# Kernel optimization log

Measured on AMD Instinct MI355X. Metric: run time of the kernel, lower is better.

Reference implementation:

```python
import jax, jax.numpy as jnp
import numpy as np

F_NHID = 64
C_NHID = 64
U_INIT = F_NHID + C_NHID + 1   # 129
U_OUT = F_NHID + C_NHID        # 128
U_HID = 128
N_AGG = 4
M_INIT = 3 * N_AGG * U_OUT + C_NHID  # 1600
M_HID = 256
M_OUT = C_NHID


def setup_inputs() -> dict:
    key = jax.random.key(0)
    ks = jax.random.split(key, 12)
    B, Nc, Nf = 4, 512, 256
    h_fac = jax.random.normal(ks[0], (B, Nf, F_NHID), dtype=jnp.float32)
    h_cus = jax.random.normal(ks[1], (B, Nc, C_NHID), dtype=jnp.float32)
    edge = jax.random.normal(ks[2], (B, Nc, Nf, 1), dtype=jnp.float32)
    adj = jax.random.randint(ks[3], (B, Nc, Nf), 0, 2).astype(jnp.float32)
    def lin(k, i, o):
        return jax.random.normal(k, (i, o), dtype=jnp.float32) / np.sqrt(i)
    return {
        'h_fac': h_fac, 'h_cus': h_cus, 'edge': edge, 'adj': adj,
        'U_W1': lin(ks[4], U_INIT, U_HID), 'U_b1': jnp.zeros((U_HID,), jnp.float32),
        'U_W2': lin(ks[5], U_HID, U_OUT), 'U_b2': jnp.zeros((U_OUT,), jnp.float32),
        'M_W1': lin(ks[6], M_INIT, M_HID), 'M_b1': jnp.zeros((M_HID,), jnp.float32),
        'M_W2': lin(ks[7], M_HID, M_OUT), 'M_b2': jnp.zeros((M_OUT,), jnp.float32),
    }


def reference(h_fac, h_cus, edge, adj, U_W1, U_b1, U_W2, U_b2, M_W1, M_b1, M_W2, M_b2):
    B, Nc, c = h_cus.shape
    Nf = h_fac.shape[1]
    # Per-edge message input: [customer_feat, facility_feat, edge_scalar] -> (B,Nc,Nf,U_INIT)
    msg = jnp.concatenate([
        jnp.broadcast_to(h_cus[:, :, None, :], (B, Nc, Nf, c)),
        jnp.broadcast_to(h_fac[:, None, :, :], (B, Nc, Nf, h_fac.shape[-1])),
        edge,
    ], axis=-1)
    # U MLP (pretransformation): relu -> linear
    m = jax.nn.relu(msg @ U_W1 + U_b1)
    m = m @ U_W2 + U_b2  # (B, Nc, Nf, U_OUT)

    mask = adj > 0                              # (B, Nc, Nf)
    maskf = mask[..., None].astype(m.dtype)     # (B, Nc, Nf, 1)
    cnt = jnp.sum(maskf, axis=2)                # (B, Nc, 1)
    mean = jnp.sum(m * maskf, axis=2) / cnt     # nanmean over masked entries
    var = jnp.sum(((m - mean[:, :, None, :]) ** 2) * maskf, axis=2) / cnt
    std = jnp.sqrt(var)                         # population std (divides by count)
    mx = jnp.max(jnp.where(mask[..., None], m, -jnp.inf), axis=2)
    mn = jnp.min(jnp.where(mask[..., None], m, jnp.inf), axis=2)

    # Degree-based scalers (get_avgd + scale_amplification/attenuation)
    deg_c = jnp.sum(adj, axis=-1)               # (B, Nc)
    deg_f = jnp.sum(adj, axis=-2)               # (B, Nf)
    avg_d = jnp.mean(jnp.concatenate([jnp.log(deg_c + 1.0), jnp.log(deg_f + 1.0)], axis=-1), axis=-1)  # (B,)
    scale = (jnp.log(deg_c + 1.0) / avg_d[:, None])[..., None]          # (B, Nc, 1)
    scale_inv = jnp.where(scale != 0, 1.0 / scale, jnp.zeros_like(scale))

    feats = [h_cus]
    for a in (mean, std, mx, mn):
        feats.extend([a, a * scale, a * scale_inv])
    h = jnp.concatenate(feats, axis=-1)         # (B, Nc, M_INIT)

    # M MLP (posttransformation): relu -> linear (last activation 'none')
    h = jax.nn.relu(h @ M_W1 + M_b1)
    out = h @ M_W2 + M_b2                       # (B, Nc, C_NHID)
    return out
```

## Files before the change

### kernel.cpp

```cpp
#include <hip/hip_runtime.h>
#include <hip/hip_bf16.h>


using bs8 = __attribute__((ext_vector_type(8))) short;
using f4  = __attribute__((ext_vector_type(4))) float;
using f2  = __attribute__((ext_vector_type(2))) float;

__device__ __forceinline__ unsigned short f2bf(float f) {
    union { float f; unsigned int u; } x; x.f = f;
    unsigned int u = x.u + 0x7FFFu + ((x.u >> 16) & 1u);
    return (unsigned short)(u >> 16);
}

__device__ __forceinline__ unsigned int pkbf(float a, float b) {
    __hip_bfloat162 h = __float22bfloat162_rn(make_float2(a, b));
    union { __hip_bfloat162 h; unsigned int u; } c; c.h = h;
    return c.u;
}

__global__ void PNALayer_35081292874189_kernel() {}

#define OFF_AC     0u
#define OFF_AF     1048576u
#define OFF_DEGC   1572864u
#define OFF_SCALE  1585152u
#define OFF_SINV   1593344u
#define OFF_FEATB  1601536u
#define OFF_HMID   8155392u
#define OFF_W2T    10252544u
#define OFF_W1TB   10318080u
#define OFF_DEGFP  11170048u
#define WS_NEED    11235584u

__global__ void PNALayer_ws_fail(float* out, int n) {
    int i = blockIdx.x * 256 + threadIdx.x;
    if (i < n) out[i] = 2500.0f;
}

__global__ void PNALayer_prep1(
    const float* h_fac, const float* h_cus, const float* adj,
    const float* U_W1, const float* U_b1, const float* U_W2, const float* M_W1,
    float* wsAc, float* wsAf, float* wsDegC,
    unsigned short* wsW2Tb, unsigned short* wsW1Tb, float* wsDegFP)
{
    __shared__ float sH[64];
    __shared__ float sRed[256];
    __shared__ float sT[64][65];
    int bid = blockIdx.x, t = threadIdx.x;

    if (bid < 1024) {
        int b = bid >> 8, f = bid & 255;
        if (t < 64) sH[t] = h_fac[(b * 256 + f) * 64 + t];
        __syncthreads();
        if (t < 128) {
            float acc = 0.f;
            for (int k = 0; k < 64; ++k)
                acc += sH[k] * U_W1[(64 + k) * 128 + t];
            wsAf[(b * 256 + f) * 128 + t] = acc;
        }
    } else if (bid < 3072) {
        int bc = bid - 1024;
        if (t < 64) sH[t] = h_cus[bc * 64 + t];
        __syncthreads();
        if (t < 128) {
            float acc = U_b1[t];
            for (int k = 0; k < 64; ++k)
                acc += sH[k] * U_W1[k * 128 + t];
            wsAc[bc * 128 + t] = acc;
        }
        float v = adj[bc * 256 + t];
        sRed[t] = v; __syncthreads();
        for (int s = 128; s > 0; s >>= 1) { if (t < s) sRed[t] += sRed[t + s]; __syncthreads(); }
        if (t == 0) wsDegC[bc] = sRed[0];
    } else if (bid < 3076) {
        int l = bid - 3072;
        int k0 = (l >> 1) * 64, n0 = (l & 1) * 64;
        for (int rep = 0; rep < 16; ++rep) {
            int idx = rep * 256 + t; int r = idx >> 6, c = idx & 63;
            sT[r][c] = U_W2[(k0 + r) * 128 + n0 + c];
        }
        __syncthreads();
        for (int rep = 0; rep < 16; ++rep) {
            int idx = rep * 256 + t; int r = idx >> 6, c = idx & 63;
            wsW2Tb[(n0 + r) * 128 + k0 + c] = f2bf(sT[c][r]);
        }
    } else if (bid < 3176) {
        int l = bid - 3076;
        int k0 = (l % 25) * 64, n0 = (l / 25) * 64;
        for (int rep = 0; rep < 16; ++rep) {
            int idx = rep * 256 + t; int r = idx >> 6, c = idx & 63;
            sT[r][c] = M_W1[(k0 + r) * 256 + n0 + c];
        }
        __syncthreads();
        for (int rep = 0; rep < 16; ++rep) {
            int idx = rep * 256 + t; int r = idx >> 6, c = idx & 63;
            wsW1Tb[(n0 + r) * 1664 + k0 + c] = f2bf(sT[c][r]);
        }
    } else if (bid < 3177) {
        for (int i = 0; i < 64; ++i) {
            int idx = i * 256 + t;
            int n = idx >> 6, k = 1600 + (idx & 63);
            wsW1Tb[n * 1664 + k] = 0;
        }
    } else {
        int l = bid - 3177;
        int b = l >> 4, ch = l & 15;
        const float* ap = adj + (b * 512 + ch * 32) * 256 + t;
        float s = 0.f;
#pragma unroll 8
        for (int c = 0; c < 32; ++c)
            s += ap[c * 256];
        wsDegFP[(b * 16 + ch) * 256 + t] = s;
    }
}

__global__ void PNALayer_prep2(
    const float* wsDegFP, const float* wsDegC, float* wsScale, float* wsSinv)
{
    __shared__ float sRed[256];
    __shared__ float sAvg;
    int b = blockIdx.x, t = threadIdx.x;
    float df = 0.f;
#pragma unroll
    for (int ch = 0; ch < 16; ++ch)
        df += wsDegFP[(b * 16 + ch) * 256 + t];
    float v = logf(wsDegC[b * 512 + t] + 1.f) + logf(wsDegC[b * 512 + t + 256] + 1.f)
            + logf(df + 1.f);
    sRed[t] = v; __syncthreads();
    for (int s = 128; s > 0; s >>= 1) { if (t < s) sRed[t] += sRed[t + s]; __syncthreads(); }
    if (t == 0) sAvg = sRed[0] / 768.f;
    __syncthreads();
    float avg = sAvg;
    for (int c = t; c < 512; c += 256) {
        float lg = logf(wsDegC[b * 512 + c] + 1.f);
        float sc = lg / avg;
        float si = (sc != 0.f) ? 1.f / sc : 0.f;
        wsScale[b * 512 + c] = sc;
        wsSinv[b * 512 + c] = si;
    }
}

__global__ __launch_bounds__(256, 4) void PNALayer_edge(
    const float* h_cus, const float* edge, const float* adj,
    const float* U_W1, const float* U_b2,
    const float* wsAc, const float* wsAf, const unsigned short* wsW2Tb,
    const float* wsScale, const float* wsSinv,
    unsigned short* featB)
{
    __shared__ __align__(16) unsigned short sM1[64 * 136];
    __shared__ float sE[256];
    __shared__ float sAc[128];
    __shared__ float sWe[128];
    __shared__ unsigned short sFidx[256];
    __shared__ unsigned long long sBal[4];

    int bc = blockIdx.x;
    int b  = bc >> 9;
    int t  = threadIdx.x;
    int w = t >> 6, quad = (t >> 4) & 3, ln = t & 15;

    int r0 = w * 32 + ln;
    int r1 = w * 32 + 16 + ln;
    bs8 bw0[4], bw1[4];
#pragma unroll
    for (int kk = 0; kk < 4; ++kk) {
        bw0[kk] = *(const bs8*)(wsW2Tb + r0 * 128 + kk * 32 + quad * 8);
        bw1[kk] = *(const bs8*)(wsW2Tb + r1 * 128 + kk * 32 + quad * 8);
    }
    float b2v0 = U_b2[r0], b2v1 = U_b2[r1];

    sE[t] = edge[bc * 256 + t];
    bool m = adj[bc * 256 + t] > 0.f;
    unsigned long long bal = __ballot(m);
    if ((t & 63) == 0) sBal[t >> 6] = bal;
    if (t < 128) {
        sAc[t] = wsAc[bc * 128 + t];
        sWe[t] = U_W1[128 * 128 + t];
    } else if (t < 192) {
        int j = t - 128;
        featB[bc * 1600 + j] = f2bf(h_cus[bc * 64 + j]);
    }
    __syncthreads();

    unsigned long long b0 = sBal[0], b1 = sBal[1], b2 = sBal[2], b3 = sBal[3];
    int cnt = __popcll(b0) + __popcll(b1) + __popcll(b2) + __popcll(b3);
    {
        int wv = t >> 6, l = t & 63;
        int base = 0;
        if (wv > 0) base += __popcll(b0);
        if (wv > 1) base += __popcll(b1);
        if (wv > 2) base += __popcll(b2);
        int rank = __popcll(bal & ((1ULL << l) - 1ULL));
        if (m) sFidx[base + rank] = (unsigned short)t;
    }
    __syncthreads();

    int ntiles = (cnt + 63) >> 6;

    f2 aS0 = (f2){0.f, 0.f}, aQ0 = (f2){0.f, 0.f};
    f2 aMx0 = (f2){-1e30f, -1e30f}, aMn0 = (f2){1e30f, 1e30f};
    f2 aS1 = (f2){0.f, 0.f}, aQ1 = (f2){0.f, 0.f};
    f2 aMx1 = (f2){-1e30f, -1e30f}, aMn1 = (f2){1e30f, 1e30f};
    const f2 zero2 = (f2){0.f, 0.f};

    for (int tl = 0; tl < ntiles; ++tl) {
#pragma unroll
        for (int i = 0; i < 8; ++i) {
            int idx = i * 256 + t;
            int fl = idx >> 5, k = (idx & 31) * 4;
            int fj = tl * 64 + fl;
            uint2 p = make_uint2(0u, 0u);
            if (fj < cnt) {
                int f = sFidx[fj];
                float4 af  = *(const float4*)(wsAf + (b * 256 + f) * 128 + k);
                float4 ac4 = *(const float4*)(sAc + k);
                float4 we4 = *(const float4*)(sWe + k);
                float e = sE[f];
                f2 e2 = (f2){e, e};
                f2 s01 = (f2){ac4.x + af.x, ac4.y + af.y};
                f2 s23 = (f2){ac4.z + af.z, ac4.w + af.w};
                s01 = __builtin_elementwise_fma(e2, (f2){we4.x, we4.y}, s01);
                s23 = __builtin_elementwise_fma(e2, (f2){we4.z, we4.w}, s23);
                f2 r01 = __builtin_elementwise_max(s01, zero2);
                f2 r23 = __builtin_elementwise_max(s23, zero2);
                p.x = pkbf(r01.x, r01.y);
                p.y = pkbf(r23.x, r23.y);
            }
            *(uint2*)(sM1 + fl * 136 + k) = p;
        }
        __syncthreads();

        f4 acc0[4], acc1[4];
#pragma unroll
        for (int rt = 0; rt < 4; ++rt) {
            acc0[rt] = (f4){0.f, 0.f, 0.f, 0.f};
            acc1[rt] = (f4){0.f, 0.f, 0.f, 0.f};
        }
#pragma unroll
        for (int kk = 0; kk < 4; ++kk) {
            int ko = kk * 32 + quad * 8;
#pragma unroll
            for (int rt = 0; rt < 4; ++rt) {
                bs8 a = *(const bs8*)(sM1 + (rt * 16 + ln) * 136 + ko);
                acc0[rt] = __builtin_amdgcn_mfma_f32_16x16x32_bf16(a, bw0[kk], acc0[rt], 0, 0, 0);
                acc1[rt] = __builtin_amdgcn_mfma_f32_16x16x32_bf16(a, bw1[kk], acc1[rt], 0, 0, 0);
            }
        }

        if (((tl + 1) << 6) <= cnt) {
#pragma unroll
            for (int rt = 0; rt < 4; ++rt) {
                f2 p01 = (f2){acc0[rt][0], acc0[rt][1]};
                f2 p23 = (f2){acc0[rt][2], acc0[rt][3]};
                aS0 = aS0 + p01;
                aS0 = aS0 + p23;
                aQ0 = __builtin_elementwise_fma(p01, p01, aQ0);
                aQ0 = __builtin_elementwise_fma(p23, p23, aQ0);
                aMx0 = __builtin_elementwise_max(aMx0, __builtin_elementwise_max(p01, p23));
                aMn0 = __builtin_elementwise_min(aMn0, __builtin_elementwise_min(p01, p23));
                f2 q01 = (f2){acc1[rt][0], acc1[rt][1]};
                f2 q23 = (f2){acc1[rt][2], acc1[rt][3]};
                aS1 = aS1 + q01;
                aS1 = aS1 + q23;
                aQ1 = __builtin_elementwise_fma(q01, q01, aQ1);
                aQ1 = __builtin_elementwise_fma(q23, q23, aQ1);
                aMx1 = __builtin_elementwise_max(aMx1, __builtin_elementwise_max(q01, q23));
                aMn1 = __builtin_elementwise_min(aMn1, __builtin_elementwise_min(q01, q23));
            }
        } else {
#pragma unroll
            for (int rt = 0; rt < 4; ++rt) {
#pragma unroll
                for (int i = 0; i < 4; ++i) {
                    int fj = tl * 64 + rt * 16 + quad * 4 + i;
                    if (fj < cnt) {
                        float v0 = acc0[rt][i];
                        aS0.x += v0;
                        aQ0.x = fmaf(v0, v0, aQ0.x);
                        aMx0.x = fmaxf(aMx0.x, v0);
                        aMn0.x = fminf(aMn0.x, v0);
                        float v1 = acc1[rt][i];
                        aS1.x += v1;
                        aQ1.x = fmaf(v1, v1, aQ1.x);
                        aMx1.x = fmaxf(aMx1.x, v1);
                        aMn1.x = fminf(aMn1.x, v1);
                    }
                }
            }
        }
        __syncthreads();
    }

    float aS[2], aQ[2], aMx[2], aMn[2];
    aS[0] = aS0.x + aS0.y;  aQ[0] = aQ0.x + aQ0.y;
    aMx[0] = fmaxf(aMx0.x, aMx0.y);  aMn[0] = fminf(aMn0.x, aMn0.y);
    aS[1] = aS1.x + aS1.y;  aQ[1] = aQ1.x + aQ1.y;
    aMx[1] = fmaxf(aMx1.x, aMx1.y);  aMn[1] = fminf(aMn1.x, aMn1.y);

#pragma unroll
    for (int ct = 0; ct < 2; ++ct) {
        aS[ct]  += __shfl_xor(aS[ct], 16, 64);  aS[ct]  += __shfl_xor(aS[ct], 32, 64);
        aQ[ct]  += __shfl_xor(aQ[ct], 16, 64);  aQ[ct]  += __shfl_xor(aQ[ct], 32, 64);
        aMx[ct] = fmaxf(aMx[ct], __shfl_xor(aMx[ct], 16, 64));
        aMx[ct] = fmaxf(aMx[ct], __shfl_xor(aMx[ct], 32, 64));
        aMn[ct] = fminf(aMn[ct], __shfl_xor(aMn[ct], 16, 64));
        aMn[ct] = fminf(aMn[ct], __shfl_xor(aMn[ct], 32, 64));
    }

    if (quad == 0) {
        float cntf = (float)cnt;
        float sc = wsScale[bc], si = wsSinv[bc];
        unsigned short* fr = featB + bc * 1600;
        float b2[2] = {b2v0, b2v1};
#pragma unroll
        for (int ct = 0; ct < 2; ++ct) {
            int col = w * 32 + ct * 16 + ln;
            float meanr = aS[ct] / cntf;
            float mean  = meanr + b2[ct];
            float var   = fmaxf(aQ[ct] / cntf - meanr * meanr, 0.f);
            float stdv  = sqrtf(var);
            float mx = aMx[ct] + b2[ct], mn = aMn[ct] + b2[ct];
            fr[64 + col]   = f2bf(mean); fr[192 + col]  = f2bf(mean * sc); fr[320 + col]  = f2bf(mean * si);
            fr[448 + col]  = f2bf(stdv); fr[576 + col]  = f2bf(stdv * sc); fr[704 + col]  = f2bf(stdv * si);
            fr[832 + col]  = f2bf(mx);   fr[960 + col]  = f2bf(mx * sc);   fr[1088 + col] = f2bf(mx * si);
            fr[1216 + col] = f2bf(mn);   fr[1344 + col] = f2bf(mn * sc);   fr[1472 + col] = f2bf(mn * si);
        }
    }
}

__global__ __launch_bounds__(512, 2) void PNALayer_mlp1(
    const unsigned short* featB, const unsigned short* wsW1Tb, const float* M_b1,
    float* h_mid)
{
    __shared__ __align__(16) unsigned short sA[32 * 136];
    __shared__ __align__(16) unsigned short sB[64 * 136];
    int t = threadIdx.x;
    int rb = (blockIdx.x >> 2) * 32, cb = (blockIdx.x & 3) * 64;
    int w = t >> 6, quad = (t >> 4) & 3, ln = t & 15;
    int wr = w >> 2, wc = w & 3;

    f4 acc = (f4){0.f, 0.f, 0.f, 0.f};

    for (int kt = 0; kt < 13; ++kt) {
        int kb = kt * 128;
        {
            int row = t >> 4, c8 = (t & 15) * 8;
            *(uint4*)(sA + row * 136 + c8) =
                *(const uint4*)(featB + (rb + row) * 1600 + kb + c8);
        }
#pragma unroll
        for (int i = 0; i < 2; ++i) {
            int vi = i * 512 + t;
            int row = vi >> 4, c8 = (vi & 15) * 8;
            *(uint4*)(sB + row * 136 + c8) =
                *(const uint4*)(wsW1Tb + (cb + row) * 1664 + kb + c8);
        }
        __syncthreads();
#pragma unroll
        for (int kk = 0; kk < 4; ++kk) {
            int ko = kk * 32 + quad * 8;
            bs8 a  = *(const bs8*)(sA + (wr * 16 + ln) * 136 + ko);
            bs8 bb = *(const bs8*)(sB + (wc * 16 + ln) * 136 + ko);
            acc = __builtin_amdgcn_mfma_f32_16x16x32_bf16(a, bb, acc, 0, 0, 0);
        }
        __syncthreads();
    }
    int col = cb + wc * 16 + ln;
    float b1v = M_b1[col];
#pragma unroll
    for (int i = 0; i < 4; ++i) {
        int row = rb + wr * 16 + quad * 4 + i;
        h_mid[row * 256 + col] = fmaxf(acc[i] + b1v, 0.f);
    }
}

__global__ void PNALayer_mlp2(
    const float* h_mid, const float* M_W2, const float* M_b2, float* out)
{
    int q = blockIdx.x * 256 + threadIdx.x;
    int row0 = q >> 6, j = q & 63;
    int row1 = row0 + 1024;
    float acc0 = M_b2[j], acc1 = acc0;
    const float* h0 = h_mid + row0 * 256;
    const float* h1 = h_mid + row1 * 256;
#pragma unroll 8
    for (int k = 0; k < 256; ++k) {
        float wv = M_W2[k * 64 + j];
        acc0 = fmaf(h0[k], wv, acc0);
        acc1 = fmaf(h1[k], wv, acc1);
    }
    out[row0 * 64 + j] = acc0;
    out[row1 * 64 + j] = acc1;
}

extern "C" void kernel_launch(void* const* d_in, const int* in_sizes, int n_in,
                              void* d_out, int out_size, void* d_ws, size_t ws_size,
                              hipStream_t stream) {
    const float* h_fac = (const float*)d_in[0];
    const float* h_cus = (const float*)d_in[1];
    const float* edge  = (const float*)d_in[2];
    const float* adj   = (const float*)d_in[3];
    const float* U_W1  = (const float*)d_in[4];
    const float* U_b1  = (const float*)d_in[5];
    const float* U_W2  = (const float*)d_in[6];
    const float* U_b2  = (const float*)d_in[7];
    const float* M_W1  = (const float*)d_in[8];
    const float* M_b1  = (const float*)d_in[9];
    const float* M_W2  = (const float*)d_in[10];
    const float* M_b2  = (const float*)d_in[11];
    (void)in_sizes; (void)n_in;

    float* outp = (float*)d_out;
    int nblk_out = (out_size + 255) / 256;

    if (ws_size < (size_t)WS_NEED) {
        PNALayer_ws_fail<<<nblk_out, 256, 0, stream>>>(outp, out_size);
        return;
    }

    char* ws = (char*)d_ws;
    float*          wsAc   = (float*)(ws + OFF_AC);
    float*          wsAf   = (float*)(ws + OFF_AF);
    float*          wsDegC = (float*)(ws + OFF_DEGC);
    float*          wsScal = (float*)(ws + OFF_SCALE);
    float*          wsSinv = (float*)(ws + OFF_SINV);
    unsigned short* wsFeatB= (unsigned short*)(ws + OFF_FEATB);
    float*          wsHmid = (float*)(ws + OFF_HMID);
    unsigned short* wsW2Tb = (unsigned short*)(ws + OFF_W2T);
    unsigned short* wsW1Tb = (unsigned short*)(ws + OFF_W1TB);
    float*          wsDegFP= (float*)(ws + OFF_DEGFP);

    PNALayer_prep1<<<3241, 256, 0, stream>>>(
        h_fac, h_cus, adj, U_W1, U_b1, U_W2, M_W1,
        wsAc, wsAf, wsDegC, wsW2Tb, wsW1Tb, wsDegFP);
    PNALayer_prep2<<<4, 256, 0, stream>>>(wsDegFP, wsDegC, wsScal, wsSinv);
    PNALayer_edge<<<2048, 256, 0, stream>>>(
        h_cus, edge, adj, U_W1, U_b2,
        wsAc, wsAf, wsW2Tb, wsScal, wsSinv, wsFeatB);
    PNALayer_mlp1<<<256, 512, 0, stream>>>(wsFeatB, wsW1Tb, M_b1, wsHmid);
    PNALayer_mlp2<<<256, 256, 0, stream>>>(wsHmid, M_W2, M_b2, outp);
}
```

Baseline: 147.8 us.

## Double-buffer edge-kernel M1 tiles and stage h_mid rows in LDS for mlp2

The edge kernel now double-buffers the bf16 hidden-activation tile in shared memory. It prefetches the next tile's wsAf rows into registers before the MFMA work on the current tile, and writes the ReLU-packed result into the other buffer afterwards, so global-load latency overlaps compute and one barrier per tile is removed. The mlp2 kernel now loads 8 rows of h_mid into LDS with coalesced float4 loads instead of each thread striding through global memory. The cost is double the sM1 LDS use and extra registers for the prefetched float4s, which may lower occupancy under launch_bounds(256,4). The mlp2 launch grid must also match the new 8-rows-per-block mapping.

```diff
diff --git a/kernel.cpp b/kernel.cpp
--- a/kernel.cpp
+++ b/kernel.cpp
@@ -147,7 +147,7 @@
     const float* wsScale, const float* wsSinv,
     unsigned short* featB)
 {
-    __shared__ __align__(16) unsigned short sM1[64 * 136];
+    __shared__ __align__(16) unsigned short sM1[2][64 * 136];
     __shared__ float sE[256];
     __shared__ float sAc[128];
     __shared__ float sWe[128];
@@ -196,22 +196,16 @@
     __syncthreads();
 
     int ntiles = (cnt + 63) >> 6;
-
-    f2 aS0 = (f2){0.f, 0.f}, aQ0 = (f2){0.f, 0.f};
-    f2 aMx0 = (f2){-1e30f, -1e30f}, aMn0 = (f2){1e30f, 1e30f};
-    f2 aS1 = (f2){0.f, 0.f}, aQ1 = (f2){0.f, 0.f};
-    f2 aMx1 = (f2){-1e30f, -1e30f}, aMn1 = (f2){1e30f, 1e30f};
     const f2 zero2 = (f2){0.f, 0.f};
 
-    for (int tl = 0; tl < ntiles; ++tl) {
+    {
 #pragma unroll
         for (int i = 0; i < 8; ++i) {
             int idx = i * 256 + t;
             int fl = idx >> 5, k = (idx & 31) * 4;
-            int fj = tl * 64 + fl;
             uint2 p = make_uint2(0u, 0u);
-            if (fj < cnt) {
-                int f = sFidx[fj];
+            if (fl < cnt) {
+                int f = sFidx[fl];
                 float4 af  = *(const float4*)(wsAf + (b * 256 + f) * 128 + k);
                 float4 ac4 = *(const float4*)(sAc + k);
                 float4 we4 = *(const float4*)(sWe + k);
@@ -226,9 +220,35 @@
                 p.x = pkbf(r01.x, r01.y);
                 p.y = pkbf(r23.x, r23.y);
             }
-            *(uint2*)(sM1 + fl * 136 + k) = p;
-        }
-        __syncthreads();
+            *(uint2*)(sM1[0] + fl * 136 + k) = p;
+        }
+    }
+    __syncthreads();
+
+    f2 aS0 = (f2){0.f, 0.f}, aQ0 = (f2){0.f, 0.f};
+    f2 aMx0 = (f2){-1e30f, -1e30f}, aMn0 = (f2){1e30f, 1e30f};
+    f2 aS1 = (f2){0.f, 0.f}, aQ1 = (f2){0.f, 0.f};
+    f2 aMx1 = (f2){-1e30f, -1e30f}, aMn1 = (f2){1e30f, 1e30f};
+
+    for (int tl = 0; tl < ntiles; ++tl) {
+        int cur = tl & 1, nxt = cur ^ 1;
+        bool have_next = (tl + 1) < ntiles;
+
+        float4 af[8]; int fxi[8];
+        if (have_next) {
+#pragma unroll
+            for (int i = 0; i < 8; ++i) {
+                int idx = i * 256 + t;
+                int fl = idx >> 5, k = (idx & 31) * 4;
+                int fj = (tl + 1) * 64 + fl;
+                fxi[i] = -1;
+                if (fj < cnt) {
+                    int f = sFidx[fj];
+                    fxi[i] = f;
+                    af[i] = *(const float4*)(wsAf + (b * 256 + f) * 128 + k);
+                }
+            }
+        }
 
         f4 acc0[4], acc1[4];
 #pragma unroll
@@ -241,7 +261,7 @@
             int ko = kk * 32 + quad * 8;
 #pragma unroll
             for (int rt = 0; rt < 4; ++rt) {
-                bs8 a = *(const bs8*)(sM1 + (rt * 16 + ln) * 136 + ko);
+                bs8 a = *(const bs8*)(sM1[cur] + (rt * 16 + ln) * 136 + ko);
                 acc0[rt] = __builtin_amdgcn_mfma_f32_16x16x32_bf16(a, bw0[kk], acc0[rt], 0, 0, 0);
                 acc1[rt] = __builtin_amdgcn_mfma_f32_16x16x32_bf16(a, bw1[kk], acc1[rt], 0, 0, 0);
             }
@@ -288,6 +308,30 @@
                 }
             }
         }
+
+        if (have_next) {
+#pragma unroll
+            for (int i = 0; i < 8; ++i) {
+                int idx = i * 256 + t;
+                int fl = idx >> 5, k = (idx & 31) * 4;
+                uint2 p = make_uint2(0u, 0u);
+                if (fxi[i] >= 0) {
+                    float4 ac4 = *(const float4*)(sAc + k);
+                    float4 we4 = *(const float4*)(sWe + k);
+                    float e = sE[fxi[i]];
+                    f2 e2 = (f2){e, e};
+                    f2 s01 = (f2){ac4.x + af[i].x, ac4.y + af[i].y};
+                    f2 s23 = (f2){ac4.z + af[i].z, ac4.w + af[i].w};
+                    s01 = __builtin_elementwise_fma(e2, (f2){we4.x, we4.y}, s01);
+                    s23 = __builtin_elementwise_fma(e2, (f2){we4.z, we4.w}, s23);
+                    f2 r01 = __builtin_elementwise_max(s01, zero2);
+                    f2 r23 = __builtin_elementwise_max(s23, zero2);
+                    p.x = pkbf(r01.x, r01.y);
+                    p.y = pkbf(r23.x, r23.y);
+                }
+                *(uint2*)(sM1[nxt] + fl * 136 + k) = p;
+            }
+        }
         __syncthreads();
     }
 
@@ -374,23 +418,32 @@
     }
 }
 
-__global__ void PNALayer_mlp2(
+__global__ __launch_bounds__(256) void PNALayer_mlp2(
     const float* h_mid, const float* M_W2, const float* M_b2, float* out)
 {
-    int q = blockIdx.x * 256 + threadIdx.x;
-    int row0 = q >> 6, j = q & 63;
-    int row1 = row0 + 1024;
+    __shared__ float sH[8 * 256];
+    int t = threadIdx.x;
+    int rb = blockIdx.x * 8;
+#pragma unroll
+    for (int i = 0; i < 2; ++i) {
+        int vi = i * 256 + t;
+        int row = vi >> 6, c4 = (vi & 63) * 4;
+        *(float4*)(sH + row * 256 + c4) =
+            *(const float4*)(h_mid + (rb + row) * 256 + c4);
+    }
+    __syncthreads();
+    int j = t & 63, r = t >> 6;
     float acc0 = M_b2[j], acc1 = acc0;
-    const float* h0 = h_mid + row0 * 256;
-    const float* h1 = h_mid + row1 * 256;
+    const float* h0 = sH + r * 256;
+    const float* h1 = sH + (r + 4) * 256;
 #pragma unroll 8
     for (int k = 0; k < 256; ++k) {
         float wv = M_W2[k * 64 + j];
         acc0 = fmaf(h0[k], wv, acc0);
         acc1 = fmaf(h1[k], wv, acc1);
     }
-    out[row0 * 64 + j] = acc0;
-    out[row1 * 64 + j] = acc1;
+    out[(rb + r) * 64 + j] = acc0;
+    out[(rb + r + 4) * 64 + j] = acc1;
 }
 
 extern "C" void kernel_launch(void* const* d_in, const int* in_sizes, int n_in,
```

Result: slower. 190.1 us (+28.6%).
